# Kernel optimization log

Measured on AMD Instinct MI355X. Metric: run time of the kernel, lower is better.

Reference implementation:

```python
import jax, jax.numpy as jnp
import numpy as np

N_NODES = 100000
N_EDGES = 1600000
IN_F = 48
EDGE_F = 32
HID_F = 128
OUT_F = 64


def seg_mean(msgs, dst, n):
    # mean over incoming edges per destination node; zero for isolated nodes (DGL semantics)
    s = jax.ops.segment_sum(msgs, dst, num_segments=n)
    deg = jax.ops.segment_sum(jnp.ones((msgs.shape[0],), msgs.dtype), dst, num_segments=n)
    return s / jnp.maximum(deg, 1.0)[:, None]


def setup_inputs() -> dict:
    key = jax.random.key(0)
    ks = jax.random.split(key, 12)
    sc = lambda fi: 1.0 / np.sqrt(fi)
    return {
        "nfeat": jax.random.normal(ks[0], (N_NODES, IN_F), jnp.float32),
        "efeat": jax.random.normal(ks[1], (N_EDGES, EDGE_F), jnp.float32),
        "src": jax.random.randint(ks[2], (N_EDGES,), 0, N_NODES, jnp.int32),
        "dst": jax.random.randint(ks[3], (N_EDGES,), 0, N_NODES, jnp.int32),
        # edge encoder: Linear(edge_feats -> in_feats)
        "We": jax.random.uniform(ks[4], (EDGE_F, IN_F), jnp.float32, -sc(EDGE_F), sc(EDGE_F)),
        "be": jnp.zeros((IN_F,), jnp.float32),
        # SAGEConv1: in = 2*in_feats -> hid ; fc_self + fc_neigh + bias
        "W1s": jax.random.uniform(ks[5], (2 * IN_F, HID_F), jnp.float32, -sc(2 * IN_F), sc(2 * IN_F)),
        "W1n": jax.random.uniform(ks[6], (2 * IN_F, HID_F), jnp.float32, -sc(2 * IN_F), sc(2 * IN_F)),
        "b1": jnp.zeros((HID_F,), jnp.float32),
        # SAGEConv2: hid -> out
        "W2s": jax.random.uniform(ks[7], (HID_F, OUT_F), jnp.float32, -sc(HID_F), sc(HID_F)),
        "W2n": jax.random.uniform(ks[8], (HID_F, OUT_F), jnp.float32, -sc(HID_F), sc(HID_F)),
        "b2": jnp.zeros((OUT_F,), jnp.float32),
    }


def reference(nfeat, efeat, src, dst, We, be, W1s, W1n, b1, W2s, W2n, b2):
    n = nfeat.shape[0]
    # edge encoder + relu
    e = jax.nn.relu(efeat @ We + be)                       # [E, in]
    # update_all(u_mul_e, mean): gather src, multiply by edge feat, mean per dst
    m = nfeat[src] * e                                     # [E, in]
    h_neigh0 = seg_mean(m, dst, n)                         # [N, in]
    h = jnp.concatenate([nfeat, h_neigh0], axis=1)         # [N, 2*in]
    # SAGEConv1 (mean): out = fc_self(h) + fc_neigh(mean_neighbors(h)) + b
    hn1 = seg_mean(h[src], dst, n)
    h1 = jax.nn.relu(h @ W1s + hn1 @ W1n + b1)             # [N, hid]
    # SAGEConv2
    hn2 = seg_mean(h1[src], dst, n)
    out = h1 @ W2s + hn2 @ W2n + b2                        # [N, out]
    return out
```

## Files before the change

kernel.cpp:

```cpp
#include <hip/hip_runtime.h>

#define IN_F 48
#define EDGE_F 32
#define HID_F 128
#define OUT_F 64



__global__ void k_hist(const int* __restrict__ dst, int* __restrict__ cnt, int E) {
    int e = blockIdx.x * 256 + threadIdx.x;
    if (e < E) atomicAdd(&cnt[dst[e]], 1);
}

__global__ void k_scan1(int* __restrict__ cnt, int* __restrict__ offsets,
                        int* __restrict__ blksum, int N) {
    __shared__ int sh[1024];
    int tid = threadIdx.x;
    int g = blockIdx.x * 1024 + tid;
    sh[tid] = (g < N) ? cnt[g] : 0;
    if (g < N) cnt[g] = 0;
    __syncthreads();
#pragma unroll
    for (int off = 1; off < 1024; off <<= 1) {
        int t = (tid >= off) ? sh[tid - off] : 0;
        __syncthreads();
        sh[tid] += t;
        __syncthreads();
    }
    if (g < N) offsets[1 + g] = sh[tid];
    if (tid == 1023) blksum[blockIdx.x] = sh[tid];
}

__global__ void k_scan2(int* __restrict__ blksum, int nb) {
    __shared__ int sh[256];
    int tid = threadIdx.x;
    int orig = (tid < nb) ? blksum[tid] : 0;
    sh[tid] = orig;
    __syncthreads();
#pragma unroll
    for (int off = 1; off < 256; off <<= 1) {
        int t = (tid >= off) ? sh[tid - off] : 0;
        __syncthreads();
        sh[tid] += t;
        __syncthreads();
    }
    if (tid < nb) blksum[tid] = sh[tid] - orig;
}

__global__ void k_scan3(int* __restrict__ offsets, const int* __restrict__ blksum, int N) {
    int g = blockIdx.x * 1024 + threadIdx.x;
    if (g < N) offsets[1 + g] += blksum[blockIdx.x];
    if (g == 0) offsets[0] = 0;
}

__global__ void k_fill(const int* __restrict__ dst, const int* __restrict__ src,
                       const int* __restrict__ offsets, int* __restrict__ cursor,
                       unsigned long long* __restrict__ pack, int E) {
    int e = blockIdx.x * 256 + threadIdx.x;
    if (e >= E) return;
    int d = dst[e];
    int s = src[e];
    int p = atomicAdd(&cursor[d], 1);
    int pos = offsets[d] + p;
    pack[pos] = ((unsigned long long)d << 42) | ((unsigned long long)s << 21) | (unsigned long long)e;
}

__global__ __launch_bounds__(256) void k_edge_reduce(
    const float* __restrict__ efeat, const float* __restrict__ nfeat,
    const unsigned long long* __restrict__ pack,
    const float* __restrict__ We, const float* __restrict__ be,
    float* __restrict__ hn0sum, int E)
{
    __shared__ float lmsg[256][49];
    __shared__ int ld[256];
    __shared__ unsigned long long hm[4];
    __shared__ int dnb[2];
    int tid = threadIdx.x;
    int B0 = blockIdx.x * 256;
    int i = B0 + tid;
    int nvalid = min(256, E - B0);
    if (tid == 0) {
        dnb[0] = (B0 > 0) ? (int)(pack[B0 - 1] >> 42) : -9;
        dnb[1] = (B0 + 256 < E) ? (int)(pack[B0 + 256] >> 42) : -9;
    }
    int d = -3;
    if (i < E) {
        unsigned long long v = pack[i];
        int e = (int)(v & 0x1FFFFF);
        int s = (int)((v >> 21) & 0x1FFFFF);
        d = (int)(v >> 42);

        float ef[EDGE_F];
        const float4* ef4 = (const float4*)(efeat + (size_t)e * EDGE_F);
#pragma unroll
        for (int q = 0; q < EDGE_F / 4; ++q) {
            float4 t = ef4[q];
            ef[4 * q + 0] = t.x; ef[4 * q + 1] = t.y; ef[4 * q + 2] = t.z; ef[4 * q + 3] = t.w;
        }
        float acc[IN_F];
#pragma unroll
        for (int j = 0; j < IN_F; ++j) acc[j] = be[j];
#pragma unroll
        for (int k = 0; k < EDGE_F; ++k) {
            float ek = ef[k];
#pragma unroll
            for (int j = 0; j < IN_F; ++j) acc[j] = fmaf(ek, We[k * IN_F + j], acc[j]);
        }
        const float4* n4 = (const float4*)(nfeat + (size_t)s * IN_F);
#pragma unroll
        for (int q = 0; q < IN_F / 4; ++q) {
            float4 nv = n4[q];
            lmsg[tid][4 * q + 0] = fmaxf(acc[4 * q + 0], 0.0f) * nv.x;
            lmsg[tid][4 * q + 1] = fmaxf(acc[4 * q + 1], 0.0f) * nv.y;
            lmsg[tid][4 * q + 2] = fmaxf(acc[4 * q + 2], 0.0f) * nv.z;
            lmsg[tid][4 * q + 3] = fmaxf(acc[4 * q + 3], 0.0f) * nv.w;
        }
    }
    ld[tid] = d;
    __syncthreads();

    bool head = (i < E) && (tid == 0 || d != ld[tid - 1]);
    unsigned long long m = __ballot(head);
    int wv = tid >> 6, lane = tid & 63;
    if (lane == 0) hm[wv] = m;
    __syncthreads();

    int dprev = dnb[0], dnext = dnb[1];
    unsigned long long mym = hm[wv];
    while (mym) {
        int rel = __ffsll(mym) - 1;
        mym &= mym - 1;
        int a = wv * 64 + rel;
        int b = nvalid;
        {
            unsigned long long mm = (rel < 63) ? (hm[wv] & (~0ULL << (rel + 1))) : 0ULL;
            int w2 = wv;
            while (true) {
                if (mm) { b = w2 * 64 + __ffsll(mm) - 1; break; }
                if (++w2 >= 4) break;
                mm = hm[w2];
            }
        }
        int dd = ld[a];
        bool cut = (a == 0 && dd == dprev) || (b == nvalid && dd == dnext);
        if (lane < IN_F) {
            float sum = 0.0f;
            for (int t = a; t < b; ++t) sum += lmsg[t][lane];
            float* dp = hn0sum + (size_t)dd * IN_F + lane;
            if (cut) atomicAdd(dp, sum);
            else *dp = sum;
        }
    }
}

__global__ void k_hcatb(const float* __restrict__ nfeat, const float* __restrict__ hn0sum,
                        const int* __restrict__ offsets, float* __restrict__ hcat, int N) {
    int idx = blockIdx.x * 256 + threadIdx.x;
    int total = N * 12;
    if (idx >= total) return;
    int node = idx / 12;
    int q = idx - node * 12;
    float4 nv = ((const float4*)nfeat)[idx];
    float4 hv = ((const float4*)hn0sum)[idx];
    int deg = offsets[node + 1] - offsets[node];
    float ivn = 1.0f / (float)max(deg, 1);
    float4* out4 = (float4*)(hcat + (size_t)node * 96);
    out4[q] = nv;
    float4 o;
    o.x = hv.x * ivn; o.y = hv.y * ivn; o.z = hv.z * ivn; o.w = hv.w * ivn;
    out4[12 + q] = o;
}

__global__ __launch_bounds__(256) void k_gather96(
    const float* __restrict__ hcat, const unsigned long long* __restrict__ pack,
    const int* __restrict__ offsets, float* __restrict__ hn1m, int N) {
    int node = blockIdx.x * 4 + (threadIdx.x >> 6);
    int j = threadIdx.x & 63;
    if (node >= N) return;
    const float* tabA = hcat + j;
    const float* tabB = hcat + 64 + j;
    int s0 = offsets[node], s1 = offsets[node + 1];
    float ivn = 1.0f / (float)max(s1 - s0, 1);
    float sA = 0.0f, sB = 0.0f;
    int i = s0;
    for (; i + 4 <= s1; i += 4) {
        int sa = (int)((pack[i] >> 21) & 0x1FFFFF);
        int sb = (int)((pack[i + 1] >> 21) & 0x1FFFFF);
        int sc = (int)((pack[i + 2] >> 21) & 0x1FFFFF);
        int sd = (int)((pack[i + 3] >> 21) & 0x1FFFFF);
        float a0 = tabA[(size_t)sa * 96], a1 = tabA[(size_t)sb * 96];
        float a2 = tabA[(size_t)sc * 96], a3 = tabA[(size_t)sd * 96];
        sA += (a0 + a1) + (a2 + a3);
        if (j < 32) {
            float b0 = tabB[(size_t)sa * 96], b1 = tabB[(size_t)sb * 96];
            float b2 = tabB[(size_t)sc * 96], b3 = tabB[(size_t)sd * 96];
            sB += (b0 + b1) + (b2 + b3);
        }
    }
    for (; i < s1; ++i) {
        int sa = (int)((pack[i] >> 21) & 0x1FFFFF);
        sA += tabA[(size_t)sa * 96];
        if (j < 32) sB += tabB[(size_t)sa * 96];
    }
    hn1m[(size_t)node * 96 + j] = sA * ivn;
    if (j < 32) hn1m[(size_t)node * 96 + 64 + j] = sB * ivn;
}

__global__ __launch_bounds__(256) void k_mm1p(
    const float* __restrict__ hcat, const float* __restrict__ hn1m,
    const float* __restrict__ W1s, const float* __restrict__ W1n,
    const float* __restrict__ b1, const float* __restrict__ W2n,
    float* __restrict__ h1, float* __restrict__ y2, int N) {
    __shared__ float xs[16][192];
    __shared__ float hs[16][128];
    int wv = threadIdx.x >> 6, lane = threadIdx.x & 63;
    int base = blockIdx.x * 16;
#pragma unroll
    for (int rr = 0; rr < 4; ++rr) {
        int row = base + wv * 4 + rr;
        int r = row < N ? row : N - 1;
#pragma unroll
        for (int kk = 0; kk < 3; ++kk) {
            int k = lane + kk * 64;
            float v = (k < 96) ? hcat[(size_t)r * 96 + k] : hn1m[(size_t)r * 96 + (k - 96)];
            xs[wv * 4 + rr][k] = v;
        }
    }
    __syncthreads();
    const float* x0 = xs[wv * 4 + 0];
    const float* x1 = xs[wv * 4 + 1];
    const float* x2 = xs[wv * 4 + 2];
    const float* x3 = xs[wv * 4 + 3];
    int c0 = lane, c1 = lane + 64;
    float a00 = b1[c0], a01 = b1[c1];
    float a10 = a00, a11 = a01, a20 = a00, a21 = a01, a30 = a00, a31 = a01;
#pragma unroll 4
    for (int k = 0; k < 96; ++k) {
        float w0 = W1s[k * 128 + c0], w1 = W1s[k * 128 + c1];
        a00 = fmaf(x0[k], w0, a00); a01 = fmaf(x0[k], w1, a01);
        a10 = fmaf(x1[k], w0, a10); a11 = fmaf(x1[k], w1, a11);
        a20 = fmaf(x2[k], w0, a20); a21 = fmaf(x2[k], w1, a21);
        a30 = fmaf(x3[k], w0, a30); a31 = fmaf(x3[k], w1, a31);
    }
#pragma unroll 4
    for (int k = 0; k < 96; ++k) {
        float w0 = W1n[k * 128 + c0], w1 = W1n[k * 128 + c1];
        a00 = fmaf(x0[96 + k], w0, a00); a01 = fmaf(x0[96 + k], w1, a01);
        a10 = fmaf(x1[96 + k], w0, a10); a11 = fmaf(x1[96 + k], w1, a11);
        a20 = fmaf(x2[96 + k], w0, a20); a21 = fmaf(x2[96 + k], w1, a21);
        a30 = fmaf(x3[96 + k], w0, a30); a31 = fmaf(x3[96 + k], w1, a31);
    }
    float accs[4][2] = {{a00, a01}, {a10, a11}, {a20, a21}, {a30, a31}};
#pragma unroll
    for (int rr = 0; rr < 4; ++rr) {
        int row = base + wv * 4 + rr;
        float v0 = fmaxf(accs[rr][0], 0.0f);
        float v1 = fmaxf(accs[rr][1], 0.0f);
        hs[wv * 4 + rr][c0] = v0;
        hs[wv * 4 + rr][c1] = v1;
        if (row < N) {
            h1[(size_t)row * 128 + c0] = v0;
            h1[(size_t)row * 128 + c1] = v1;
        }
    }
    const float* p0 = hs[wv * 4 + 0];
    const float* p1 = hs[wv * 4 + 1];
    const float* p2 = hs[wv * 4 + 2];
    const float* p3 = hs[wv * 4 + 3];
    float q0 = 0.0f, q1 = 0.0f, q2 = 0.0f, q3 = 0.0f;
#pragma unroll 4
    for (int k = 0; k < 128; ++k) {
        float w = W2n[k * 64 + lane];
        q0 = fmaf(p0[k], w, q0); q1 = fmaf(p1[k], w, q1);
        q2 = fmaf(p2[k], w, q2); q3 = fmaf(p3[k], w, q3);
    }
    float qs[4] = {q0, q1, q2, q3};
#pragma unroll
    for (int rr = 0; rr < 4; ++rr) {
        int row = base + wv * 4 + rr;
        if (row < N) y2[(size_t)row * 64 + lane] = qs[rr];
    }
}

__global__ __launch_bounds__(256) void k_gather64(
    const float* __restrict__ y2, const unsigned long long* __restrict__ pack,
    const int* __restrict__ offsets, float* __restrict__ hn2p, int N) {
    int node = blockIdx.x * 4 + (threadIdx.x >> 6);
    int j = threadIdx.x & 63;
    if (node >= N) return;
    int s0 = offsets[node], s1 = offsets[node + 1];
    float ivn = 1.0f / (float)max(s1 - s0, 1);
    float sum = 0.0f;
    int i = s0;
    for (; i + 4 <= s1; i += 4) {
        int sa = (int)((pack[i] >> 21) & 0x1FFFFF);
        int sb = (int)((pack[i + 1] >> 21) & 0x1FFFFF);
        int sc = (int)((pack[i + 2] >> 21) & 0x1FFFFF);
        int sd = (int)((pack[i + 3] >> 21) & 0x1FFFFF);
        float va = y2[(size_t)sa * 64 + j];
        float vb = y2[(size_t)sb * 64 + j];
        float vc = y2[(size_t)sc * 64 + j];
        float vd = y2[(size_t)sd * 64 + j];
        sum += (va + vb) + (vc + vd);
    }
    for (; i < s1; ++i) sum += y2[(size_t)((pack[i] >> 21) & 0x1FFFFF) * 64 + j];
    hn2p[(size_t)node * 64 + j] = sum * ivn;
}

__global__ __launch_bounds__(256) void k_mm2b(
    const float* __restrict__ h1, const float* __restrict__ hn2p,
    const float* __restrict__ W2s, const float* __restrict__ b2,
    float* __restrict__ out, int N) {
    __shared__ float xs[16][128];
    int wv = threadIdx.x >> 6, lane = threadIdx.x & 63;
    int base = blockIdx.x * 16;
#pragma unroll
    for (int rr = 0; rr < 4; ++rr) {
        int row = base + wv * 4 + rr;
        int r = row < N ? row : N - 1;
        xs[wv * 4 + rr][lane]      = h1[(size_t)r * 128 + lane];
        xs[wv * 4 + rr][lane + 64] = h1[(size_t)r * 128 + lane + 64];
    }
    __syncthreads();
    const float* x0 = xs[wv * 4 + 0];
    const float* x1 = xs[wv * 4 + 1];
    const float* x2 = xs[wv * 4 + 2];
    const float* x3 = xs[wv * 4 + 3];
    float a0 = b2[lane], a1 = a0, a2 = a0, a3 = a0;
#pragma unroll 4
    for (int k = 0; k < 128; ++k) {
        float w = W2s[k * 64 + lane];
        a0 = fmaf(x0[k], w, a0); a1 = fmaf(x1[k], w, a1);
        a2 = fmaf(x2[k], w, a2); a3 = fmaf(x3[k], w, a3);
    }
    float accs[4] = {a0, a1, a2, a3};
#pragma unroll
    for (int rr = 0; rr < 4; ++rr) {
        int row = base + wv * 4 + rr;
        if (row < N) out[(size_t)row * 64 + lane] = accs[rr] + hn2p[(size_t)row * 64 + lane];
    }
}

extern "C" void kernel_launch(void* const* d_in, const int* in_sizes, int n_in,
                              void* d_out, int out_size, void* d_ws, size_t ws_size,
                              hipStream_t stream) {
    const float* nfeat = (const float*)d_in[0];
    const float* efeat = (const float*)d_in[1];
    const int*   src   = (const int*)d_in[2];
    const int*   dst   = (const int*)d_in[3];
    const float* We    = (const float*)d_in[4];
    const float* be    = (const float*)d_in[5];
    const float* W1s   = (const float*)d_in[6];
    const float* W1n   = (const float*)d_in[7];
    const float* b1    = (const float*)d_in[8];
    const float* W2s   = (const float*)d_in[9];
    const float* W2n   = (const float*)d_in[10];
    const float* b2    = (const float*)d_in[11];
    float* out = (float*)d_out;

    int N = in_sizes[0] / IN_F;
    int E = in_sizes[2];

    int*                cursor  = (int*)d_ws;
    float*              hn0sum  = (float*)(cursor + N);
    int*                offsets = (int*)(hn0sum + (size_t)48 * N);
    int*                blksum  = offsets + N + 64;
    unsigned long long* pack    = (unsigned long long*)(blksum + 256);
    float*              hcat    = (float*)(pack + E);
    float*              h1      = hcat + (size_t)96 * N;
    float*              y2      = h1 + (size_t)128 * N;
    float*              hn1m    = y2 + (size_t)64 * N;
    float*              hn2p    = hn1m + (size_t)96 * N;

    int nb = (N + 1023) / 1024;

    (void)hipMemsetAsync(cursor, 0, (size_t)49 * N * sizeof(float), stream);
    k_hist<<<(E + 255) / 256, 256, 0, stream>>>(dst, cursor, E);
    k_scan1<<<nb, 1024, 0, stream>>>(cursor, offsets, blksum, N);
    k_scan2<<<1, 256, 0, stream>>>(blksum, nb);
    k_scan3<<<nb, 1024, 0, stream>>>(offsets, blksum, N);

    k_fill<<<(E + 255) / 256, 256, 0, stream>>>(dst, src, offsets, cursor, pack, E);
    k_edge_reduce<<<(E + 255) / 256, 256, 0, stream>>>(efeat, nfeat, pack, We, be, hn0sum, E);
    k_hcatb<<<(N * 12 + 255) / 256, 256, 0, stream>>>(nfeat, hn0sum, offsets, hcat, N);
    k_gather96<<<(N + 3) / 4, 256, 0, stream>>>(hcat, pack, offsets, hn1m, N);
    k_mm1p<<<(N + 15) / 16, 256, 0, stream>>>(hcat, hn1m, W1s, W1n, b1, W2n, h1, y2, N);
    k_gather64<<<(N + 3) / 4, 256, 0, stream>>>(y2, pack, offsets, hn2p, N);
    k_mm2b<<<(N + 15) / 16, 256, 0, stream>>>(h1, hn2p, W2s, b2, out, N);
}
```

Before: 895.3 us.

## Fuse neighbor gathers into matmul kernels and split edge encoder into halves

The two neighbor-mean gather kernels are folded into the two matmul kernels, so the gathered rows go straight into shared memory or registers and never make a global-memory round trip through hn1m/hn2p. The edge-reduce kernel now computes the edge encoder in two 24-column halves, halving the shared message buffer and the per-thread accumulator array, which is meant to raise occupancy. The cost is an extra pass of segment scanning and syncs in edge_reduce. The fused matmul kernels also run a serialized per-row gather before the GEMM, so fewer threads may be in flight to hide gather latency.

```diff
diff --git a/kernel.cpp b/kernel.cpp
--- a/kernel.cpp
+++ b/kernel.cpp
@@ -71,7 +71,7 @@
     const float* __restrict__ We, const float* __restrict__ be,
     float* __restrict__ hn0sum, int E)
 {
-    __shared__ float lmsg[256][49];
+    __shared__ float lmsg[256][25];
     __shared__ int ld[256];
     __shared__ unsigned long long hm[4];
     __shared__ int dnb[2];
@@ -83,37 +83,18 @@
         dnb[0] = (B0 > 0) ? (int)(pack[B0 - 1] >> 42) : -9;
         dnb[1] = (B0 + 256 < E) ? (int)(pack[B0 + 256] >> 42) : -9;
     }
-    int d = -3;
+    int d = -3, s = 0;
+    float ef[EDGE_F];
     if (i < E) {
         unsigned long long v = pack[i];
         int e = (int)(v & 0x1FFFFF);
-        int s = (int)((v >> 21) & 0x1FFFFF);
+        s = (int)((v >> 21) & 0x1FFFFF);
         d = (int)(v >> 42);
-
-        float ef[EDGE_F];
         const float4* ef4 = (const float4*)(efeat + (size_t)e * EDGE_F);
 #pragma unroll
         for (int q = 0; q < EDGE_F / 4; ++q) {
             float4 t = ef4[q];
             ef[4 * q + 0] = t.x; ef[4 * q + 1] = t.y; ef[4 * q + 2] = t.z; ef[4 * q + 3] = t.w;
-        }
-        float acc[IN_F];
-#pragma unroll
-        for (int j = 0; j < IN_F; ++j) acc[j] = be[j];
-#pragma unroll
-        for (int k = 0; k < EDGE_F; ++k) {
-            float ek = ef[k];
-#pragma unroll
-            for (int j = 0; j < IN_F; ++j) acc[j] = fmaf(ek, We[k * IN_F + j], acc[j]);
-        }
-        const float4* n4 = (const float4*)(nfeat + (size_t)s * IN_F);
-#pragma unroll
-        for (int q = 0; q < IN_F / 4; ++q) {
-            float4 nv = n4[q];
-            lmsg[tid][4 * q + 0] = fmaxf(acc[4 * q + 0], 0.0f) * nv.x;
-            lmsg[tid][4 * q + 1] = fmaxf(acc[4 * q + 1], 0.0f) * nv.y;
-            lmsg[tid][4 * q + 2] = fmaxf(acc[4 * q + 2], 0.0f) * nv.z;
-            lmsg[tid][4 * q + 3] = fmaxf(acc[4 * q + 3], 0.0f) * nv.w;
         }
     }
     ld[tid] = d;
@@ -125,31 +106,60 @@
     if (lane == 0) hm[wv] = m;
     __syncthreads();
 
-    int dprev = dnb[0], dnext = dnb[1];
-    unsigned long long mym = hm[wv];
-    while (mym) {
-        int rel = __ffsll(mym) - 1;
-        mym &= mym - 1;
-        int a = wv * 64 + rel;
-        int b = nvalid;
-        {
-            unsigned long long mm = (rel < 63) ? (hm[wv] & (~0ULL << (rel + 1))) : 0ULL;
-            int w2 = wv;
-            while (true) {
-                if (mm) { b = w2 * 64 + __ffsll(mm) - 1; break; }
-                if (++w2 >= 4) break;
-                mm = hm[w2];
-            }
-        }
-        int dd = ld[a];
-        bool cut = (a == 0 && dd == dprev) || (b == nvalid && dd == dnext);
-        if (lane < IN_F) {
-            float sum = 0.0f;
-            for (int t = a; t < b; ++t) sum += lmsg[t][lane];
-            float* dp = hn0sum + (size_t)dd * IN_F + lane;
-            if (cut) atomicAdd(dp, sum);
-            else *dp = sum;
-        }
+#pragma unroll
+    for (int c = 0; c < 2; ++c) {
+        if (i < E) {
+            float acc[24];
+#pragma unroll
+            for (int j = 0; j < 24; ++j) acc[j] = be[c * 24 + j];
+#pragma unroll
+            for (int k = 0; k < EDGE_F; ++k) {
+                float ek = ef[k];
+#pragma unroll
+                for (int j = 0; j < 24; ++j)
+                    acc[j] = fmaf(ek, We[k * IN_F + c * 24 + j], acc[j]);
+            }
+            const float4* n4 = (const float4*)(nfeat + (size_t)s * IN_F + c * 24);
+#pragma unroll
+            for (int q = 0; q < 6; ++q) {
+                float4 nv = n4[q];
+                lmsg[tid][4 * q + 0] = fmaxf(acc[4 * q + 0], 0.0f) * nv.x;
+                lmsg[tid][4 * q + 1] = fmaxf(acc[4 * q + 1], 0.0f) * nv.y;
+                lmsg[tid][4 * q + 2] = fmaxf(acc[4 * q + 2], 0.0f) * nv.z;
+                lmsg[tid][4 * q + 3] = fmaxf(acc[4 * q + 3], 0.0f) * nv.w;
+            }
+        }
+        __syncthreads();
+
+        int dprev = dnb[0], dnext = dnb[1];
+        unsigned long long mym = hm[wv];
+        while (mym) {
+            int rel = __ffsll(mym) - 1;
+            mym &= mym - 1;
+            int a = wv * 64 + rel;
+            int b = nvalid;
+            {
+                unsigned long long mm = (rel < 63) ? (hm[wv] & (~0ULL << (rel + 1))) : 0ULL;
+                int w2 = wv;
+                while (true) {
+                    if (mm) { b = w2 * 64 + __ffsll(mm) - 1; break; }
+                    if (++w2 >= 4) break;
+                    mm = hm[w2];
+                }
+            }
+            int dd = ld[a];
+            bool cut = (a == 0 && dd == dprev) || (b == nvalid && dd == dnext);
+            if (lane < 24) {
+                float sum = 0.0f;
+                int t = a;
+                for (; t + 2 <= b; t += 2) sum += lmsg[t][lane] + lmsg[t + 1][lane];
+                if (t < b) sum += lmsg[t][lane];
+                float* dp = hn0sum + (size_t)dd * IN_F + c * 24 + lane;
+                if (cut) atomicAdd(dp, sum);
+                else *dp = sum;
+            }
+        }
+        __syncthreads();
     }
 }
 
@@ -171,43 +181,9 @@
     out4[12 + q] = o;
 }
 
-__global__ __launch_bounds__(256) void k_gather96(
-    const float* __restrict__ hcat, const unsigned long long* __restrict__ pack,
-    const int* __restrict__ offsets, float* __restrict__ hn1m, int N) {
-    int node = blockIdx.x * 4 + (threadIdx.x >> 6);
-    int j = threadIdx.x & 63;
-    if (node >= N) return;
-    const float* tabA = hcat + j;
-    const float* tabB = hcat + 64 + j;
-    int s0 = offsets[node], s1 = offsets[node + 1];
-    float ivn = 1.0f / (float)max(s1 - s0, 1);
-    float sA = 0.0f, sB = 0.0f;
-    int i = s0;
-    for (; i + 4 <= s1; i += 4) {
-        int sa = (int)((pack[i] >> 21) & 0x1FFFFF);
-        int sb = (int)((pack[i + 1] >> 21) & 0x1FFFFF);
-        int sc = (int)((pack[i + 2] >> 21) & 0x1FFFFF);
-        int sd = (int)((pack[i + 3] >> 21) & 0x1FFFFF);
-        float a0 = tabA[(size_t)sa * 96], a1 = tabA[(size_t)sb * 96];
-        float a2 = tabA[(size_t)sc * 96], a3 = tabA[(size_t)sd * 96];
-        sA += (a0 + a1) + (a2 + a3);
-        if (j < 32) {
-            float b0 = tabB[(size_t)sa * 96], b1 = tabB[(size_t)sb * 96];
-            float b2 = tabB[(size_t)sc * 96], b3 = tabB[(size_t)sd * 96];
-            sB += (b0 + b1) + (b2 + b3);
-        }
-    }
-    for (; i < s1; ++i) {
-        int sa = (int)((pack[i] >> 21) & 0x1FFFFF);
-        sA += tabA[(size_t)sa * 96];
-        if (j < 32) sB += tabB[(size_t)sa * 96];
-    }
-    hn1m[(size_t)node * 96 + j] = sA * ivn;
-    if (j < 32) hn1m[(size_t)node * 96 + 64 + j] = sB * ivn;
-}
-
 __global__ __launch_bounds__(256) void k_mm1p(
-    const float* __restrict__ hcat, const float* __restrict__ hn1m,
+    const float* __restrict__ hcat,
+    const unsigned long long* __restrict__ pack, const int* __restrict__ offsets,
     const float* __restrict__ W1s, const float* __restrict__ W1n,
     const float* __restrict__ b1, const float* __restrict__ W2n,
     float* __restrict__ h1, float* __restrict__ y2, int N) {
@@ -215,16 +191,39 @@
     __shared__ float hs[16][128];
     int wv = threadIdx.x >> 6, lane = threadIdx.x & 63;
     int base = blockIdx.x * 16;
+    const float* tabA = hcat + lane;
+    const float* tabB = hcat + 64 + lane;
 #pragma unroll
     for (int rr = 0; rr < 4; ++rr) {
         int row = base + wv * 4 + rr;
         int r = row < N ? row : N - 1;
-#pragma unroll
-        for (int kk = 0; kk < 3; ++kk) {
-            int k = lane + kk * 64;
-            float v = (k < 96) ? hcat[(size_t)r * 96 + k] : hn1m[(size_t)r * 96 + (k - 96)];
-            xs[wv * 4 + rr][k] = v;
-        }
+        xs[wv * 4 + rr][lane] = hcat[(size_t)r * 96 + lane];
+        if (lane < 32) xs[wv * 4 + rr][64 + lane] = hcat[(size_t)r * 96 + 64 + lane];
+        int s0 = offsets[r], s1 = offsets[r + 1];
+        float ivn = 1.0f / (float)max(s1 - s0, 1);
+        float sA = 0.0f, sB = 0.0f;
+        int i = s0;
+        for (; i + 4 <= s1; i += 4) {
+            int sa = (int)((pack[i] >> 21) & 0x1FFFFF);
+            int sb = (int)((pack[i + 1] >> 21) & 0x1FFFFF);
+            int sc = (int)((pack[i + 2] >> 21) & 0x1FFFFF);
+            int sd = (int)((pack[i + 3] >> 21) & 0x1FFFFF);
+            float a0 = tabA[(size_t)sa * 96], a1 = tabA[(size_t)sb * 96];
+            float a2 = tabA[(size_t)sc * 96], a3 = tabA[(size_t)sd * 96];
+            sA += (a0 + a1) + (a2 + a3);
+            if (lane < 32) {
+                float b0 = tabB[(size_t)sa * 96], b1v = tabB[(size_t)sb * 96];
+                float b2v = tabB[(size_t)sc * 96], b3 = tabB[(size_t)sd * 96];
+                sB += (b0 + b1v) + (b2v + b3);
+            }
+        }
+        for (; i < s1; ++i) {
+            int sa = (int)((pack[i] >> 21) & 0x1FFFFF);
+            sA += tabA[(size_t)sa * 96];
+            if (lane < 32) sB += tabB[(size_t)sa * 96];
+        }
+        xs[wv * 4 + rr][96 + lane] = sA * ivn;
+        if (lane < 32) xs[wv * 4 + rr][160 + lane] = sB * ivn;
     }
     __syncthreads();
     const float* x0 = xs[wv * 4 + 0];
@@ -282,44 +281,38 @@
     }
 }
 
-__global__ __launch_bounds__(256) void k_gather64(
-    const float* __restrict__ y2, const unsigned long long* __restrict__ pack,
-    const int* __restrict__ offsets, float* __restrict__ hn2p, int N) {
-    int node = blockIdx.x * 4 + (threadIdx.x >> 6);
-    int j = threadIdx.x & 63;
-    if (node >= N) return;
-    int s0 = offsets[node], s1 = offsets[node + 1];
-    float ivn = 1.0f / (float)max(s1 - s0, 1);
-    float sum = 0.0f;
-    int i = s0;
-    for (; i + 4 <= s1; i += 4) {
-        int sa = (int)((pack[i] >> 21) & 0x1FFFFF);
-        int sb = (int)((pack[i + 1] >> 21) & 0x1FFFFF);
-        int sc = (int)((pack[i + 2] >> 21) & 0x1FFFFF);
-        int sd = (int)((pack[i + 3] >> 21) & 0x1FFFFF);
-        float va = y2[(size_t)sa * 64 + j];
-        float vb = y2[(size_t)sb * 64 + j];
-        float vc = y2[(size_t)sc * 64 + j];
-        float vd = y2[(size_t)sd * 64 + j];
-        sum += (va + vb) + (vc + vd);
-    }
-    for (; i < s1; ++i) sum += y2[(size_t)((pack[i] >> 21) & 0x1FFFFF) * 64 + j];
-    hn2p[(size_t)node * 64 + j] = sum * ivn;
-}
-
 __global__ __launch_bounds__(256) void k_mm2b(
-    const float* __restrict__ h1, const float* __restrict__ hn2p,
+    const float* __restrict__ h1, const float* __restrict__ y2,
+    const unsigned long long* __restrict__ pack, const int* __restrict__ offsets,
     const float* __restrict__ W2s, const float* __restrict__ b2,
     float* __restrict__ out, int N) {
     __shared__ float xs[16][128];
     int wv = threadIdx.x >> 6, lane = threadIdx.x & 63;
     int base = blockIdx.x * 16;
+    float gs[4];
 #pragma unroll
     for (int rr = 0; rr < 4; ++rr) {
         int row = base + wv * 4 + rr;
         int r = row < N ? row : N - 1;
         xs[wv * 4 + rr][lane]      = h1[(size_t)r * 128 + lane];
         xs[wv * 4 + rr][lane + 64] = h1[(size_t)r * 128 + lane + 64];
+        int s0 = offsets[r], s1 = offsets[r + 1];
+        float ivn = 1.0f / (float)max(s1 - s0, 1);
+        float sum = 0.0f;
+        int i = s0;
+        for (; i + 4 <= s1; i += 4) {
+            int sa = (int)((pack[i] >> 21) & 0x1FFFFF);
+            int sb = (int)((pack[i + 1] >> 21) & 0x1FFFFF);
+            int sc = (int)((pack[i + 2] >> 21) & 0x1FFFFF);
+            int sd = (int)((pack[i + 3] >> 21) & 0x1FFFFF);
+            float va = y2[(size_t)sa * 64 + lane];
+            float vb = y2[(size_t)sb * 64 + lane];
+            float vc = y2[(size_t)sc * 64 + lane];
+            float vd = y2[(size_t)sd * 64 + lane];
+            sum += (va + vb) + (vc + vd);
+        }
+        for (; i < s1; ++i) sum += y2[(size_t)((pack[i] >> 21) & 0x1FFFFF) * 64 + lane];
+        gs[rr] = sum * ivn;
     }
     __syncthreads();
     const float* x0 = xs[wv * 4 + 0];
@@ -337,7 +330,7 @@
 #pragma unroll
     for (int rr = 0; rr < 4; ++rr) {
         int row = base + wv * 4 + rr;
-        if (row < N) out[(size_t)row * 64 + lane] = accs[rr] + hn2p[(size_t)row * 64 + lane];
+        if (row < N) out[(size_t)row * 64 + lane] = accs[rr] + gs[rr];
     }
 }
 
@@ -369,8 +362,6 @@
     float*              hcat    = (float*)(pack + E);
     float*              h1      = hcat + (size_t)96 * N;
     float*              y2      = h1 + (size_t)128 * N;
-    float*              hn1m    = y2 + (size_t)64 * N;
-    float*              hn2p    = hn1m + (size_t)96 * N;
 
     int nb = (N + 1023) / 1024;
 
@@ -383,8 +374,6 @@
     k_fill<<<(E + 255) / 256, 256, 0, stream>>>(dst, src, offsets, cursor, pack, E);
     k_edge_reduce<<<(E + 255) / 256, 256, 0, stream>>>(efeat, nfeat, pack, We, be, hn0sum, E);
     k_hcatb<<<(N * 12 + 255) / 256, 256, 0, stream>>>(nfeat, hn0sum, offsets, hcat, N);
-    k_gather96<<<(N + 3) / 4, 256, 0, stream>>>(hcat, pack, offsets, hn1m, N);
-    k_mm1p<<<(N + 15) / 16, 256, 0, stream>>>(hcat, hn1m, W1s, W1n, b1, W2n, h1, y2, N);
-    k_gather64<<<(N + 3) / 4, 256, 0, stream>>>(y2, pack, offsets, hn2p, N);
-    k_mm2b<<<(N + 15) / 16, 256, 0, stream>>>(h1, hn2p, W2s, b2, out, N);
-}
+    k_mm1p<<<(N + 15) / 16, 256, 0, stream>>>(hcat, pack, offsets, W1s, W1n, b1, W2n, h1, y2, N);
+    k_mm2b<<<(N + 15) / 16, 256, 0, stream>>>(h1, y2, pack, offsets, W2s, b2, out, N);
+}
```

After: 902.4 us. Within noise of the previous version (+0.8%).
